# Optimization experiments

Hardware: AMD Instinct MI355X
Metric: run time of the kernel (lower is better)

## Reference

```python
import jax, jax.numpy as jnp
import numpy as np

D_MODEL = 1024
NHEAD = 16
HEAD_DIM = D_MODEL // NHEAD


def setup_inputs() -> dict:
    key = jax.random.key(0)
    ks = jax.random.split(key, 11)
    B, S = 2, 2048
    scale = 1.0 / np.sqrt(D_MODEL)
    inp = {
        "query": jax.random.normal(ks[0], (B, S, D_MODEL), jnp.float32),
        "key": jax.random.normal(ks[1], (B, S, D_MODEL), jnp.float32),
        "value": jax.random.normal(ks[2], (B, S, D_MODEL), jnp.float32),
        "Wq": jax.random.normal(ks[3], (D_MODEL, D_MODEL), jnp.float32) * scale,
        "bq": jnp.zeros((D_MODEL,), jnp.float32),
        "Wk": jax.random.normal(ks[4], (D_MODEL, D_MODEL), jnp.float32) * scale,
        "bk": jnp.zeros((D_MODEL,), jnp.float32),
        "Wv": jax.random.normal(ks[5], (D_MODEL, D_MODEL), jnp.float32) * scale,
        "bv": jnp.zeros((D_MODEL,), jnp.float32),
        "Wo": jax.random.normal(ks[6], (D_MODEL, D_MODEL), jnp.float32) * scale,
        "bo": jnp.zeros((D_MODEL,), jnp.float32),
    }
    return inp


def reference(query, key, value, Wq, bq, Wk, bk, Wv, bv, Wo, bo):
    B, S, _ = query.shape
    # Linear projections (torch Linear: x @ W.T + b)
    def proj(x, W, b):
        y = x @ W.T + b
        return y.reshape(B, -1, NHEAD, HEAD_DIM).transpose(0, 2, 1, 3)  # [B,H,S,hd]
    q = proj(query, Wq, bq)
    k = proj(key, Wk, bk)
    v = proj(value, Wv, bv)
    scores = jnp.einsum("bhqd,bhkd->bhqk", q, k) / np.sqrt(HEAD_DIM)
    attn = jax.nn.softmax(scores, axis=-1)  # dropout is identity (eval / p=0)
    out = jnp.einsum("bhqk,bhkd->bhqd", attn, v)
    out = out.transpose(0, 2, 1, 3).reshape(B, S, D_MODEL)
    return out @ Wo.T + bo
```

## Files before the change

kernel.cpp:

```cpp
#include <hip/hip_runtime.h>
#include <stdint.h>

typedef __attribute__((ext_vector_type(8))) short bf16x8;
typedef __attribute__((ext_vector_type(4))) short bf16x4;
typedef __attribute__((ext_vector_type(4))) float f32x4;
typedef __attribute__((ext_vector_type(2))) unsigned int u32x2;
typedef __attribute__((ext_vector_type(4))) unsigned int u32x4;
typedef unsigned int u32;
typedef unsigned short u16;

#define S_LEN 2048
#define DMODEL 1024
#define HD 64


static __device__ __forceinline__ u16 f2bf(float f) {
  u32 u = __builtin_bit_cast(u32, f);
  return (u16)((u + 0x7fffu + ((u >> 16) & 1u)) >> 16);
}

static __device__ __forceinline__ u32 cvt_pk(float a, float b) {
  u32 r;
  asm("v_cvt_pk_bf16_f32 %0, %1, %2" : "=v"(r) : "v"(a), "v"(b));
  return r;
}

static __device__ __forceinline__ void gl_lds16(const u16* g, u16* l) {
  __builtin_amdgcn_global_load_lds((const __attribute__((address_space(1))) u32*)g,
                                   (__attribute__((address_space(3))) u32*)l, 16, 0, 0);
}

static __device__ __forceinline__ u32 lds_addr(const void* p) {
  return (u32)(uint64_t)p;
}

static __device__ __forceinline__ bf16x4 tr16(u32 addr) {
  bf16x4 r;
  asm volatile("ds_read_b64_tr_b16 %0, %1" : "=v"(r) : "v"(addr));
  return r;
}

__global__ __launch_bounds__(256) void convert_w(
    const float* __restrict__ wq, const float* __restrict__ wk,
    const float* __restrict__ wv, const float* __restrict__ wo,
    u16* __restrict__ dst) {
  size_t i = ((size_t)blockIdx.x * 256 + threadIdx.x) * 8;
  u32 wsel = (u32)((i >> 20) & 3u);
  const float* src = (wsel == 0) ? wq : (wsel == 1) ? wk : (wsel == 2) ? wv : wo;
  size_t off = i & 0xFFFFFu;
  float4 a = *(const float4*)(src + off);
  float4 b = *(const float4*)(src + off + 4);
  bf16x8 o;
  o[0] = (short)f2bf(a.x); o[1] = (short)f2bf(a.y);
  o[2] = (short)f2bf(a.z); o[3] = (short)f2bf(a.w);
  o[4] = (short)f2bf(b.x); o[5] = (short)f2bf(b.y);
  o[6] = (short)f2bf(b.z); o[7] = (short)f2bf(b.w);
  *(bf16x8*)(dst + i) = o;
}

template <int OUT_BF16, int BN>
static __device__ __forceinline__ void gemm_core(
    const u16* __restrict__ A, const u16* __restrict__ Bm,
    const float* __restrict__ bias, void* __restrict__ Y, float scale,
    int bm, int bn, u16* As, u16* Bs) {
  const int tid = threadIdx.x;
  const int lane = tid & 63, w = tid >> 6;
  const int wm = w >> 1, wn = w & 1;
  const int g = lane >> 4, l15 = lane & 15;
  constexpr int NFR = BN / 64 * 2;

  f32x4 acc[4][NFR] = {};

  const int r0 = tid >> 2, k8 = (tid & 3) * 8;
  const int r1 = (tid + 256) >> 2;
  const size_t arow0 = (size_t)(bm * 128 + r0) * DMODEL + k8;
  const size_t arow1 = (size_t)(bm * 128 + r1) * DMODEL + k8;
  const size_t brow0 = (size_t)(bn * BN + r0) * DMODEL + k8;
  const size_t brow1 = (size_t)(bn * BN + r1) * DMODEL + k8;

  auto stage = [&](int buf, int kt) {
    const int kb = kt * 32;
    u16* asb = As + buf * 4096;
    u16* bsb = Bs + buf * (BN * 32);
    gl_lds16(A + arow0 + kb, asb + w * 512);
    gl_lds16(A + arow1 + kb, asb + w * 512 + 2048);
    gl_lds16(Bm + brow0 + kb, bsb + w * 512);
    if constexpr (BN == 128) gl_lds16(Bm + brow1 + kb, bsb + w * 512 + 2048);
  };

  stage(0, 0);
  __syncthreads();
  int cur = 0;
  for (int kt = 0; kt < 32; ++kt) {
    if (kt < 31) stage(cur ^ 1, kt + 1);
    const u16* as = As + cur * 4096;
    const u16* bs = Bs + cur * (BN * 32);
    bf16x8 a[4], b[NFR];
#pragma unroll
    for (int mi = 0; mi < 4; ++mi)
      a[mi] = *(const bf16x8*)&as[(wm * 64 + mi * 16 + l15) * 32 + g * 8];
#pragma unroll
    for (int ni = 0; ni < NFR; ++ni)
      b[ni] = *(const bf16x8*)&bs[(wn * (BN / 2) + ni * 16 + l15) * 32 + g * 8];
#pragma unroll
    for (int mi = 0; mi < 4; ++mi)
#pragma unroll
      for (int ni = 0; ni < NFR; ++ni)
        acc[mi][ni] = __builtin_amdgcn_mfma_f32_16x16x32_bf16(a[mi], b[ni], acc[mi][ni], 0, 0, 0);
    __syncthreads();
    cur ^= 1;
  }

#pragma unroll
  for (int ni = 0; ni < NFR; ++ni) {
    const int col = bn * BN + wn * (BN / 2) + ni * 16 + l15;
    const float bv = bias[col];
#pragma unroll
    for (int mi = 0; mi < 4; ++mi) {
      const int row0 = bm * 128 + wm * 64 + mi * 16 + g * 4;
#pragma unroll
      for (int r = 0; r < 4; ++r) {
        float v = (acc[mi][ni][r] + bv) * scale;
        if (OUT_BF16)
          ((u16*)Y)[(size_t)(row0 + r) * DMODEL + col] = f2bf(v);
        else
          ((float*)Y)[(size_t)(row0 + r) * DMODEL + col] = v;
      }
    }
  }
}

__global__ __launch_bounds__(256) void qkv_gemm(
    const float* __restrict__ xq, const float* __restrict__ xk, const float* __restrict__ xv,
    const u16* __restrict__ W,
    const float* __restrict__ bq, const float* __restrict__ bk, const float* __restrict__ bv,
    u16* __restrict__ Qp, u16* __restrict__ Kpp, u16* __restrict__ Vpp, float qscale) {
  __shared__ u16 As[2 * 4096];
  __shared__ u16 Bs[2 * 4096];
  const int sel = blockIdx.x >> 8;
  const int bb = blockIdx.x & 255;
  const int bm = (bb & 7) * 4 + (bb >> 6);
  const int bn = (bb >> 3) & 7;
  const float* A = (sel == 0) ? xq : (sel == 1) ? xk : xv;
  const u16* Bm = W + (size_t)sel * (1024 * 1024);
  const float* bias = (sel == 0) ? bq : (sel == 1) ? bk : bv;
  u16* Y = (sel == 0) ? Qp : (sel == 1) ? Kpp : Vpp;
  const float scale = (sel == 0) ? qscale : 1.0f;

  const int tid = threadIdx.x;
  const int lane = tid & 63, w = tid >> 6;
  const int wm = w >> 1, wn = w & 1;
  const int g = lane >> 4, l15 = lane & 15;

  f32x4 acc[4][4] = {};

  const int r0 = tid >> 2, k8 = (tid & 3) * 8;
  const int r1 = (tid + 256) >> 2;
  const size_t arow0 = (size_t)(bm * 128 + r0) * DMODEL + k8;
  const size_t arow1 = (size_t)(bm * 128 + r1) * DMODEL + k8;
  const size_t brow0 = (size_t)(bn * 128 + r0) * DMODEL + k8;
  const size_t brow1 = (size_t)(bn * 128 + r1) * DMODEL + k8;

  float4 af0, af1, af2, af3;
  auto loadA = [&](int kt) {
    const int kb = kt * 32;
    af0 = *(const float4*)(A + arow0 + kb);
    af1 = *(const float4*)(A + arow0 + kb + 4);
    af2 = *(const float4*)(A + arow1 + kb);
    af3 = *(const float4*)(A + arow1 + kb + 4);
  };
  auto writeA = [&](int buf) {
    u16* asb = As + buf * 4096;
    u32x4 p0 = {cvt_pk(af0.x, af0.y), cvt_pk(af0.z, af0.w),
                cvt_pk(af1.x, af1.y), cvt_pk(af1.z, af1.w)};
    u32x4 p1 = {cvt_pk(af2.x, af2.y), cvt_pk(af2.z, af2.w),
                cvt_pk(af3.x, af3.y), cvt_pk(af3.z, af3.w)};
    *(u32x4*)(asb + tid * 8) = p0;
    *(u32x4*)(asb + tid * 8 + 2048) = p1;
  };
  auto stageB = [&](int buf, int kt) {
    const int kb = kt * 32;
    u16* bsb = Bs + buf * 4096;
    gl_lds16(Bm + brow0 + kb, bsb + w * 512);
    gl_lds16(Bm + brow1 + kb, bsb + w * 512 + 2048);
  };

  loadA(0);
  stageB(0, 0);
  writeA(0);
  __syncthreads();
  int cur = 0;
  for (int kt = 0; kt < 32; ++kt) {
    if (kt < 31) {
      loadA(kt + 1);
      stageB(cur ^ 1, kt + 1);
    }
    const u16* as = As + cur * 4096;
    const u16* bs = Bs + cur * 4096;
    bf16x8 a[4], b[4];
#pragma unroll
    for (int mi = 0; mi < 4; ++mi)
      a[mi] = *(const bf16x8*)&as[(wm * 64 + mi * 16 + l15) * 32 + g * 8];
#pragma unroll
    for (int ni = 0; ni < 4; ++ni)
      b[ni] = *(const bf16x8*)&bs[(wn * 64 + ni * 16 + l15) * 32 + g * 8];
#pragma unroll
    for (int mi = 0; mi < 4; ++mi)
#pragma unroll
      for (int ni = 0; ni < 4; ++ni)
        acc[mi][ni] = __builtin_amdgcn_mfma_f32_16x16x32_bf16(a[mi], b[ni], acc[mi][ni], 0, 0, 0);
    if (kt < 31) writeA(cur ^ 1);
    __syncthreads();
    cur ^= 1;
  }

#pragma unroll
  for (int ni = 0; ni < 4; ++ni) {
    const int col = bn * 128 + wn * 64 + ni * 16 + l15;
    const float bv = bias[col];
#pragma unroll
    for (int mi = 0; mi < 4; ++mi) {
      const int row0 = bm * 128 + wm * 64 + mi * 16 + g * 4;
#pragma unroll
      for (int r = 0; r < 4; ++r) {
        float v = (acc[mi][ni][r] + bv) * scale;
        ((u16*)Y)[(size_t)(row0 + r) * DMODEL + col] = f2bf(v);
      }
    }
  }
}

__global__ __launch_bounds__(256) void wo_gemm(
    const u16* __restrict__ A, const u16* __restrict__ Bm,
    const float* __restrict__ bias, float* __restrict__ Y) {
  __shared__ u16 As[2 * 4096];
  __shared__ u16 Bs[2 * 2048];
  const int idx = blockIdx.x;
  const int bm = (idx & 7) * 4 + (idx >> 7);
  const int bn = (idx >> 3) & 15;
  gemm_core<0, 64>(A, Bm, bias, Y, 1.0f, bm, bn, As, Bs);
}

__global__ __launch_bounds__(512, 4) void attn_fwd(
    const u16* __restrict__ Qp, const u16* __restrict__ Kp,
    const u16* __restrict__ Vp, u16* __restrict__ Op) {
  __shared__ u16 smem[32768];
  u16* Kl = smem;
  u16* Vl = smem + 8192;
  const int tid = threadIdx.x;
  const int lane = tid & 63, w = tid >> 6;
  const int g = lane >> 4, l15 = lane & 15;
  const int qs = w & 3, hf = w >> 2;
  const int bh = blockIdx.x >> 4;
  const int qt = blockIdx.x & 15;
  const int b = bh >> 4, h = bh & 15;
  const size_t rowbase = (size_t)b * S_LEN;
  const int hcol = h * HD;

  bf16x8 qf[2][2];
#pragma unroll
  for (int qb = 0; qb < 2; ++qb) {
    const int qrow = qt * 128 + qs * 32 + qb * 16 + l15;
    qf[qb][0] = *(const bf16x8*)(Qp + (rowbase + qrow) * DMODEL + hcol + g * 8);
    qf[qb][1] = *(const bf16x8*)(Qp + (rowbase + qrow) * DMODEL + hcol + 32 + g * 8);
  }

  f32x4 o[2][4] = {};
  float lsum[2] = {0.0f, 0.0f};

  const u32 sbase = lds_addr(smem);

  const int half_s = tid >> 8;
  const int kvs = (tid >> 3) & 31, slot = (tid & 7) ^ (kvs & 7);
  const size_t koff = (rowbase + half_s * 1024 + kvs) * (size_t)DMODEL + hcol + slot * 8;
  const int cc = tid & 255;
  const int hh = cc & 1, p = (cc >> 1) & 15, sub = (cc >> 5) & 1, dt0 = (cc >> 6) & 3;
  const int kvv = 8 * (p >> 2) + sub * 4 + (p & 3);
  const size_t voff = (rowbase + half_s * 1024 + kvv) * (size_t)DMODEL + hcol + dt0 * 16 + hh * 8;

  auto stage = [&](int buf, int it) {
    const size_t adv = (size_t)it * 32 * DMODEL;
    gl_lds16(Kp + koff + adv, Kl + buf * 4096 + w * 512);
    gl_lds16(Vp + voff + adv, Vl + buf * 4096 + w * 512);
  };

  stage(0, 0);
  __syncthreads();
  int cur = 0;
  for (int it = 0; it < 32; ++it) {
    if (it < 31) stage(cur ^ 1, it + 1);
    const char* kb = (const char*)smem + cur * 8192 + hf * 4096;
    const u32 vbb = sbase + 16384 + (u32)(cur * 8192 + hf * 4096);
    const u32 pswz = (u32)((l15 & 7) << 4);

    f32x4 s[2][2];
    __builtin_amdgcn_s_setprio(1);
#pragma unroll
    for (int t = 0; t < 2; ++t) {
      const int kvl = t * 16 + l15;
      const u32 swz = (u32)((kvl & 7) << 4);
      bf16x8 k0 = *(const bf16x8*)(kb + (((u32)(kvl * 128 + g * 16)) ^ swz));
      bf16x8 k1 = *(const bf16x8*)(kb + (((u32)(kvl * 128 + 64 + g * 16)) ^ swz));
      f32x4 z = {};
      s[0][t] = __builtin_amdgcn_mfma_f32_16x16x32_bf16(
          k1, qf[0][1], __builtin_amdgcn_mfma_f32_16x16x32_bf16(k0, qf[0][0], z, 0, 0, 0), 0, 0, 0);
      s[1][t] = __builtin_amdgcn_mfma_f32_16x16x32_bf16(
          k1, qf[1][1], __builtin_amdgcn_mfma_f32_16x16x32_bf16(k0, qf[1][0], z, 0, 0, 0), 0, 0, 0);
    }
    __builtin_amdgcn_s_setprio(0);

#pragma unroll
    for (int qb = 0; qb < 2; ++qb) {
      const u32 pb = (u32)(32768 + (w * 2 + qb) * 2048 + l15 * 128);
      float psum = 0.0f;
#pragma unroll
      for (int t = 0; t < 2; ++t) {
        float e0 = __builtin_amdgcn_exp2f(s[qb][t][0]);
        float e1 = __builtin_amdgcn_exp2f(s[qb][t][1]);
        float e2 = __builtin_amdgcn_exp2f(s[qb][t][2]);
        float e3 = __builtin_amdgcn_exp2f(s[qb][t][3]);
        psum += (e0 + e1) + (e2 + e3);
        u32x2 pk = {cvt_pk(e0, e1), cvt_pk(e2, e3)};
        *(u32x2*)((char*)smem + ((pb + (u32)(t * 32 + g * 8)) ^ pswz)) = pk;
      }
      lsum[qb] += psum;
    }

    bf16x8 pf[2];
    bf16x4 tv[4][2];
#pragma unroll
    for (int qb = 0; qb < 2; ++qb) {
      const u32 pb = (u32)(32768 + (w * 2 + qb) * 2048 + l15 * 128);
      pf[qb] = *(const bf16x8*)((const char*)smem + ((pb + (u32)(g * 16)) ^ pswz));
    }
#pragma unroll
    for (int dt = 0; dt < 4; ++dt)
#pragma unroll
      for (int sb = 0; sb < 2; ++sb)
        tv[dt][sb] = tr16(vbb + (u32)((dt * 2 + sb) * 512 + lane * 8));
    asm volatile("s_waitcnt lgkmcnt(0)" ::: "memory");
    __builtin_amdgcn_sched_barrier(0);
    __builtin_amdgcn_s_setprio(1);
#pragma unroll
    for (int dt = 0; dt < 4; ++dt) {
      bf16x8 vf;
      vf[0] = tv[dt][0][0]; vf[1] = tv[dt][0][1];
      vf[2] = tv[dt][0][2]; vf[3] = tv[dt][0][3];
      vf[4] = tv[dt][1][0]; vf[5] = tv[dt][1][1];
      vf[6] = tv[dt][1][2]; vf[7] = tv[dt][1][3];
      o[0][dt] = __builtin_amdgcn_mfma_f32_16x16x32_bf16(pf[0], vf, o[0][dt], 0, 0, 0);
      o[1][dt] = __builtin_amdgcn_mfma_f32_16x16x32_bf16(pf[1], vf, o[1][dt], 0, 0, 0);
    }
    __builtin_amdgcn_s_setprio(0);
    __syncthreads();
    cur ^= 1;
  }

  float ls[2];
#pragma unroll
  for (int qb = 0; qb < 2; ++qb) {
    float v = lsum[qb];
    v += __shfl_xor(v, 16);
    v += __shfl_xor(v, 32);
    ls[qb] = v;
  }
  if (w >= 4) {
    char* ob = (char*)smem + (w - 4) * 8192 + lane * 16;
#pragma unroll
    for (int qb = 0; qb < 2; ++qb)
#pragma unroll
      for (int dt = 0; dt < 4; ++dt)
        *(f32x4*)(ob + (qb * 4 + dt) * 1024) = o[qb][dt];
    float2 lw = {ls[0], ls[1]};
    *(float2*)((char*)smem + 32768 + (w - 4) * 512 + lane * 8) = lw;
  }
  __syncthreads();
  if (w < 4) {
    const char* ob = (const char*)smem + w * 8192 + lane * 16;
#pragma unroll
    for (int qb = 0; qb < 2; ++qb)
#pragma unroll
      for (int dt = 0; dt < 4; ++dt)
        o[qb][dt] += *(const f32x4*)(ob + (qb * 4 + dt) * 1024);
    const float2 lp = *(const float2*)((const char*)smem + 32768 + w * 512 + lane * 8);
    ls[0] += lp.x;
    ls[1] += lp.y;
#pragma unroll
    for (int qb = 0; qb < 2; ++qb) {
      const float linv = 1.0f / ls[qb];
      const float li0 = __shfl(linv, g * 4 + 0);
      const float li1 = __shfl(linv, g * 4 + 1);
      const float li2 = __shfl(linv, g * 4 + 2);
      const float li3 = __shfl(linv, g * 4 + 3);
      const float li[4] = {li0, li1, li2, li3};
#pragma unroll
      for (int dt = 0; dt < 4; ++dt)
#pragma unroll
        for (int r = 0; r < 4; ++r) {
          const int qr = qt * 128 + w * 32 + qb * 16 + g * 4 + r;
          Op[(rowbase + qr) * DMODEL + hcol + dt * 16 + l15] = f2bf(o[qb][dt][r] * li[r]);
        }
    }
  }
}

extern "C" void kernel_launch(void* const* d_in, const int* in_sizes, int n_in,
                              void* d_out, int out_size, void* d_ws, size_t ws_size,
                              hipStream_t stream) {
  const float* xq = (const float*)d_in[0];
  const float* xk = (const float*)d_in[1];
  const float* xv = (const float*)d_in[2];
  const float* Wq = (const float*)d_in[3];
  const float* bq = (const float*)d_in[4];
  const float* Wk = (const float*)d_in[5];
  const float* bk = (const float*)d_in[6];
  const float* Wv = (const float*)d_in[7];
  const float* bv = (const float*)d_in[8];
  const float* Wo = (const float*)d_in[9];
  const float* bo = (const float*)d_in[10];

  u16* ws = (u16*)d_ws;
  const size_t MB4 = 4096ull * 1024ull;
  u16* WQb = ws + 3 * MB4;
  u16* Qp = ws + 4 * MB4;
  u16* Kpp = ws + 5 * MB4;
  u16* Vpp = ws + 6 * MB4;
  u16* Opp = ws + 7 * MB4;

  convert_w<<<2048, 256, 0, stream>>>(Wq, Wk, Wv, Wo, WQb);

  const float qscale = 0.125f * 1.44269504088896340736f;
  qkv_gemm<<<768, 256, 0, stream>>>(xq, xk, xv, WQb, bq, bk, bv, Qp, Kpp, Vpp, qscale);

  attn_fwd<<<512, 512, 0, stream>>>(Qp, Kpp, Vpp, Opp);

  wo_gemm<<<512, 256, 0, stream>>>(Opp, WQb + 3 * 1024 * 1024, bo, (float*)d_out);
}
```

Before: 115.9 us.

## Switch attention to 32x32x16 MFMA and keep P in registers via permlane swap

Rewrites the attention inner loop to use 32x32x16 bf16 MFMAs instead of 16x16x32. The softmax probabilities are rearranged into the A-operand layout with v_permlane32_swap rather than a round-trip through LDS. This removes the P write/read to shared memory and halves the LDS footprint, which could allow higher occupancy. The V staging layout and the final reduction/epilogue are re-derived for the new fragment layout, which adds risk of layout mistakes and higher accumulator register pressure.

```diff
diff --git a/kernel.cpp b/kernel.cpp
--- a/kernel.cpp
+++ b/kernel.cpp
@@ -4,6 +4,7 @@
 typedef __attribute__((ext_vector_type(8))) short bf16x8;
 typedef __attribute__((ext_vector_type(4))) short bf16x4;
 typedef __attribute__((ext_vector_type(4))) float f32x4;
+typedef __attribute__((ext_vector_type(16))) float f32x16;
 typedef __attribute__((ext_vector_type(2))) unsigned int u32x2;
 typedef __attribute__((ext_vector_type(4))) unsigned int u32x4;
 typedef unsigned int u32;
@@ -244,12 +245,10 @@
 __global__ __launch_bounds__(512, 4) void attn_fwd(
     const u16* __restrict__ Qp, const u16* __restrict__ Kp,
     const u16* __restrict__ Vp, u16* __restrict__ Op) {
-  __shared__ u16 smem[32768];
-  u16* Kl = smem;
-  u16* Vl = smem + 8192;
+  __shared__ u16 smem[16384];
   const int tid = threadIdx.x;
   const int lane = tid & 63, w = tid >> 6;
-  const int g = lane >> 4, l15 = lane & 15;
+  const int hi = lane >> 5, l31 = lane & 31;
   const int qs = w & 3, hf = w >> 2;
   const int bh = blockIdx.x >> 4;
   const int qt = blockIdx.x & 15;
@@ -257,149 +256,144 @@
   const size_t rowbase = (size_t)b * S_LEN;
   const int hcol = h * HD;
 
-  bf16x8 qf[2][2];
-#pragma unroll
-  for (int qb = 0; qb < 2; ++qb) {
-    const int qrow = qt * 128 + qs * 32 + qb * 16 + l15;
-    qf[qb][0] = *(const bf16x8*)(Qp + (rowbase + qrow) * DMODEL + hcol + g * 8);
-    qf[qb][1] = *(const bf16x8*)(Qp + (rowbase + qrow) * DMODEL + hcol + 32 + g * 8);
-  }
-
-  f32x4 o[2][4] = {};
-  float lsum[2] = {0.0f, 0.0f};
+  bf16x8 qf[4];
+  {
+    const size_t qoff = (rowbase + qt * 128 + qs * 32 + l31) * DMODEL + hcol + hi * 8;
+#pragma unroll
+    for (int dblk = 0; dblk < 4; ++dblk)
+      qf[dblk] = *(const bf16x8*)(Qp + qoff + dblk * 16);
+  }
+
+  f32x16 o0 = {}, o1 = {};
+  float lsum = 0.0f;
 
   const u32 sbase = lds_addr(smem);
 
   const int half_s = tid >> 8;
   const int kvs = (tid >> 3) & 31, slot = (tid & 7) ^ (kvs & 7);
   const size_t koff = (rowbase + half_s * 1024 + kvs) * (size_t)DMODEL + hcol + slot * 8;
-  const int cc = tid & 255;
-  const int hh = cc & 1, p = (cc >> 1) & 15, sub = (cc >> 5) & 1, dt0 = (cc >> 6) & 3;
-  const int kvv = 8 * (p >> 2) + sub * 4 + (p & 3);
-  const size_t voff = (rowbase + half_s * 1024 + kvv) * (size_t)DMODEL + hcol + dt0 * 16 + hh * 8;
+  const int cv = tid & 255;
+  const int cc2 = cv & 1, jj = (cv >> 1) & 3, dh_s = (cv >> 3) & 1,
+            kvg_s = (cv >> 4) & 7, db_s = (cv >> 7) & 1;
+  const size_t voff = (rowbase + half_s * 1024 + kvg_s * 4 + jj) * (size_t)DMODEL
+                      + hcol + db_s * 32 + dh_s * 16 + cc2 * 8;
 
   auto stage = [&](int buf, int it) {
     const size_t adv = (size_t)it * 32 * DMODEL;
-    gl_lds16(Kp + koff + adv, Kl + buf * 4096 + w * 512);
-    gl_lds16(Vp + voff + adv, Vl + buf * 4096 + w * 512);
+    gl_lds16(Kp + koff + adv, smem + buf * 8192 + w * 512);
+    gl_lds16(Vp + voff + adv, smem + buf * 8192 + 4096 + w * 512);
   };
 
   stage(0, 0);
   __syncthreads();
   int cur = 0;
+  const int dh = (lane >> 4) & 1, c15 = lane & 15;
   for (int it = 0; it < 32; ++it) {
     if (it < 31) stage(cur ^ 1, it + 1);
-    const char* kb = (const char*)smem + cur * 8192 + hf * 4096;
-    const u32 vbb = sbase + 16384 + (u32)(cur * 8192 + hf * 4096);
-    const u32 pswz = (u32)((l15 & 7) << 4);
-
-    f32x4 s[2][2];
+    const char* kb = (const char*)smem + cur * 16384 + hf * 4096;
+    const u32 vb = sbase + (u32)(cur * 16384 + 8192 + hf * 4096);
+
+    f32x16 sA = {};
     __builtin_amdgcn_s_setprio(1);
 #pragma unroll
-    for (int t = 0; t < 2; ++t) {
-      const int kvl = t * 16 + l15;
-      const u32 swz = (u32)((kvl & 7) << 4);
-      bf16x8 k0 = *(const bf16x8*)(kb + (((u32)(kvl * 128 + g * 16)) ^ swz));
-      bf16x8 k1 = *(const bf16x8*)(kb + (((u32)(kvl * 128 + 64 + g * 16)) ^ swz));
-      f32x4 z = {};
-      s[0][t] = __builtin_amdgcn_mfma_f32_16x16x32_bf16(
-          k1, qf[0][1], __builtin_amdgcn_mfma_f32_16x16x32_bf16(k0, qf[0][0], z, 0, 0, 0), 0, 0, 0);
-      s[1][t] = __builtin_amdgcn_mfma_f32_16x16x32_bf16(
-          k1, qf[1][1], __builtin_amdgcn_mfma_f32_16x16x32_bf16(k0, qf[1][0], z, 0, 0, 0), 0, 0, 0);
+    for (int dblk = 0; dblk < 4; ++dblk) {
+      const u32 sl = (u32)((dblk * 2 + hi) ^ (l31 & 7));
+      bf16x8 kf = *(const bf16x8*)(kb + l31 * 128 + sl * 16);
+      sA = __builtin_amdgcn_mfma_f32_32x32x16_bf16(kf, qf[dblk], sA, 0, 0, 0);
     }
     __builtin_amdgcn_s_setprio(0);
 
-#pragma unroll
-    for (int qb = 0; qb < 2; ++qb) {
-      const u32 pb = (u32)(32768 + (w * 2 + qb) * 2048 + l15 * 128);
-      float psum = 0.0f;
-#pragma unroll
-      for (int t = 0; t < 2; ++t) {
-        float e0 = __builtin_amdgcn_exp2f(s[qb][t][0]);
-        float e1 = __builtin_amdgcn_exp2f(s[qb][t][1]);
-        float e2 = __builtin_amdgcn_exp2f(s[qb][t][2]);
-        float e3 = __builtin_amdgcn_exp2f(s[qb][t][3]);
-        psum += (e0 + e1) + (e2 + e3);
-        u32x2 pk = {cvt_pk(e0, e1), cvt_pk(e2, e3)};
-        *(u32x2*)((char*)smem + ((pb + (u32)(t * 32 + g * 8)) ^ pswz)) = pk;
-      }
-      lsum[qb] += psum;
-    }
-
-    bf16x8 pf[2];
-    bf16x4 tv[4][2];
-#pragma unroll
-    for (int qb = 0; qb < 2; ++qb) {
-      const u32 pb = (u32)(32768 + (w * 2 + qb) * 2048 + l15 * 128);
-      pf[qb] = *(const bf16x8*)((const char*)smem + ((pb + (u32)(g * 16)) ^ pswz));
-    }
-#pragma unroll
-    for (int dt = 0; dt < 4; ++dt)
-#pragma unroll
-      for (int sb = 0; sb < 2; ++sb)
-        tv[dt][sb] = tr16(vbb + (u32)((dt * 2 + sb) * 512 + lane * 8));
+    u32 w0[4], w1[4];
+    float psum = 0.0f;
+#pragma unroll
+    for (int bq = 0; bq < 4; ++bq) {
+      float e0 = __builtin_amdgcn_exp2f(sA[4 * bq + 0]);
+      float e1 = __builtin_amdgcn_exp2f(sA[4 * bq + 1]);
+      float e2 = __builtin_amdgcn_exp2f(sA[4 * bq + 2]);
+      float e3 = __builtin_amdgcn_exp2f(sA[4 * bq + 3]);
+      psum += (e0 + e1) + (e2 + e3);
+      w0[bq] = cvt_pk(e0, e1);
+      w1[bq] = cvt_pk(e2, e3);
+    }
+    psum += __shfl_xor(psum, 32);
+    lsum += psum;
+
+    bf16x8 pa[2];
+#pragma unroll
+    for (int kblk = 0; kblk < 2; ++kblk) {
+      u32 xa = w0[2 * kblk], ya = w0[2 * kblk + 1];
+      asm("v_permlane32_swap_b32 %0, %1" : "+v"(xa), "+v"(ya));
+      u32 xb = w1[2 * kblk], yb = w1[2 * kblk + 1];
+      asm("v_permlane32_swap_b32 %0, %1" : "+v"(xb), "+v"(yb));
+      u32x4 pw = {xa, xb, ya, yb};
+      pa[kblk] = __builtin_bit_cast(bf16x8, pw);
+    }
+
+    bf16x4 tv[2][2][2];
+#pragma unroll
+    for (int dblk = 0; dblk < 2; ++dblk)
+#pragma unroll
+      for (int kblk = 0; kblk < 2; ++kblk)
+#pragma unroll
+        for (int r = 0; r < 2; ++r)
+          tv[dblk][kblk][r] =
+              tr16(vb + (u32)(dblk * 2048 + (4 * kblk + 2 * hi + r) * 256 + dh * 128 + c15 * 8));
     asm volatile("s_waitcnt lgkmcnt(0)" ::: "memory");
     __builtin_amdgcn_sched_barrier(0);
     __builtin_amdgcn_s_setprio(1);
 #pragma unroll
-    for (int dt = 0; dt < 4; ++dt) {
-      bf16x8 vf;
-      vf[0] = tv[dt][0][0]; vf[1] = tv[dt][0][1];
-      vf[2] = tv[dt][0][2]; vf[3] = tv[dt][0][3];
-      vf[4] = tv[dt][1][0]; vf[5] = tv[dt][1][1];
-      vf[6] = tv[dt][1][2]; vf[7] = tv[dt][1][3];
-      o[0][dt] = __builtin_amdgcn_mfma_f32_16x16x32_bf16(pf[0], vf, o[0][dt], 0, 0, 0);
-      o[1][dt] = __builtin_amdgcn_mfma_f32_16x16x32_bf16(pf[1], vf, o[1][dt], 0, 0, 0);
+    for (int kblk = 0; kblk < 2; ++kblk) {
+      bf16x8 vf0, vf1;
+#pragma unroll
+      for (int j = 0; j < 4; ++j) {
+        vf0[j] = tv[0][kblk][0][j]; vf0[4 + j] = tv[0][kblk][1][j];
+        vf1[j] = tv[1][kblk][0][j]; vf1[4 + j] = tv[1][kblk][1][j];
+      }
+      o0 = __builtin_amdgcn_mfma_f32_32x32x16_bf16(pa[kblk], vf0, o0, 0, 0, 0);
+      o1 = __builtin_amdgcn_mfma_f32_32x32x16_bf16(pa[kblk], vf1, o1, 0, 0, 0);
     }
     __builtin_amdgcn_s_setprio(0);
     __syncthreads();
     cur ^= 1;
   }
 
-  float ls[2];
-#pragma unroll
-  for (int qb = 0; qb < 2; ++qb) {
-    float v = lsum[qb];
-    v += __shfl_xor(v, 16);
-    v += __shfl_xor(v, 32);
-    ls[qb] = v;
-  }
+  float* smf = (float*)smem;
+  if (w >= 4 && lane < 32) smf[(w - 4) * 32 + lane] = lsum;
+  __syncthreads();
+  float linv = 0.0f;
+  if (w < 4) linv = 1.0f / (lsum + smf[w * 32 + l31]);
+  __syncthreads();
   if (w >= 4) {
-    char* ob = (char*)smem + (w - 4) * 8192 + lane * 16;
-#pragma unroll
-    for (int qb = 0; qb < 2; ++qb)
-#pragma unroll
-      for (int dt = 0; dt < 4; ++dt)
-        *(f32x4*)(ob + (qb * 4 + dt) * 1024) = o[qb][dt];
-    float2 lw = {ls[0], ls[1]};
-    *(float2*)((char*)smem + 32768 + (w - 4) * 512 + lane * 8) = lw;
+    char* ob = (char*)smem + (w - 4) * 8192;
+#pragma unroll
+    for (int q4 = 0; q4 < 4; ++q4) {
+      f32x4 v0 = {o0[4 * q4 + 0], o0[4 * q4 + 1], o0[4 * q4 + 2], o0[4 * q4 + 3]};
+      f32x4 v1 = {o1[4 * q4 + 0], o1[4 * q4 + 1], o1[4 * q4 + 2], o1[4 * q4 + 3]};
+      *(f32x4*)(ob + q4 * 1024 + lane * 16) = v0;
+      *(f32x4*)(ob + (4 + q4) * 1024 + lane * 16) = v1;
+    }
   }
   __syncthreads();
   if (w < 4) {
-    const char* ob = (const char*)smem + w * 8192 + lane * 16;
-#pragma unroll
-    for (int qb = 0; qb < 2; ++qb)
-#pragma unroll
-      for (int dt = 0; dt < 4; ++dt)
-        o[qb][dt] += *(const f32x4*)(ob + (qb * 4 + dt) * 1024);
-    const float2 lp = *(const float2*)((const char*)smem + 32768 + w * 512 + lane * 8);
-    ls[0] += lp.x;
-    ls[1] += lp.y;
-#pragma unroll
-    for (int qb = 0; qb < 2; ++qb) {
-      const float linv = 1.0f / ls[qb];
-      const float li0 = __shfl(linv, g * 4 + 0);
-      const float li1 = __shfl(linv, g * 4 + 1);
-      const float li2 = __shfl(linv, g * 4 + 2);
-      const float li3 = __shfl(linv, g * 4 + 3);
-      const float li[4] = {li0, li1, li2, li3};
-#pragma unroll
-      for (int dt = 0; dt < 4; ++dt)
-#pragma unroll
-        for (int r = 0; r < 4; ++r) {
-          const int qr = qt * 128 + w * 32 + qb * 16 + g * 4 + r;
-          Op[(rowbase + qr) * DMODEL + hcol + dt * 16 + l15] = f2bf(o[qb][dt][r] * li[r]);
-        }
+    const char* ob = (const char*)smem + w * 8192;
+    float li[16];
+#pragma unroll
+    for (int r = 0; r < 16; ++r) {
+      const int qr = (r & 3) + 8 * (r >> 2) + 4 * hi;
+      li[r] = __shfl(linv, qr);
+    }
+#pragma unroll
+    for (int q4 = 0; q4 < 4; ++q4) {
+      f32x4 p0 = *(const f32x4*)(ob + q4 * 1024 + lane * 16);
+      f32x4 p1 = *(const f32x4*)(ob + (4 + q4) * 1024 + lane * 16);
+#pragma unroll
+      for (int j = 0; j < 4; ++j) {
+        const int r = 4 * q4 + j;
+        const int qr = (r & 3) + 8 * (r >> 2) + 4 * hi;
+        const size_t orow = (rowbase + qt * 128 + qs * 32 + qr) * DMODEL + hcol;
+        Op[orow + l31] = f2bf((o0[r] + p0[j]) * li[r]);
+        Op[orow + 32 + l31] = f2bf((o1[r] + p1[j]) * li[r]);
+      }
     }
   }
 }
```

Result: no change. 117.8 us (+1.7%).
